# Optimization experiments

Hardware: AMD Instinct MI355X
Metric: run time of the kernel (lower is better)

Reference implementation:

```python
import jax, jax.numpy as jnp
import numpy as np

D_MODEL = 1024
NUM_HEADS = 16
HEAD_DIM = D_MODEL // NUM_HEADS


def setup_inputs() -> dict:
    key = jax.random.key(0)
    k_x, k_wqkv, k_bqkv, k_wout, k_bout = jax.random.split(key, 5)
    B, S = 2, 2048
    x = jax.random.normal(k_x, (B, S, D_MODEL), dtype=jnp.float32)
    # haiku Linear: y = x @ W + b, W shape [in, out]
    init_scale = 1.0 / np.sqrt(D_MODEL)
    W_qkv = jax.random.normal(k_wqkv, (D_MODEL, 3 * D_MODEL), dtype=jnp.float32) * init_scale
    b_qkv = jnp.zeros((3 * D_MODEL,), dtype=jnp.float32)
    W_out = jax.random.normal(k_wout, (D_MODEL, D_MODEL), dtype=jnp.float32) * init_scale
    b_out = jnp.zeros((D_MODEL,), dtype=jnp.float32)
    return {"x": x, "W_qkv": W_qkv, "b_qkv": b_qkv, "W_out": W_out, "b_out": b_out}


def reference(x, W_qkv, b_qkv, W_out, b_out):
    B, S, _ = x.shape
    qkv = x @ W_qkv + b_qkv                      # [B, S, 3*D]
    q, k, v = jnp.split(qkv, 3, axis=-1)         # each [B, S, D]
    # [B, S, D] -> [B, H, S, Hd]
    def heads(t):
        return t.reshape(B, S, NUM_HEADS, HEAD_DIM).transpose(0, 2, 1, 3)
    q, k, v = heads(q), heads(k), heads(v)
    scale = jnp.sqrt(jnp.float32(HEAD_DIM)).astype(x.dtype)
    attn = jnp.einsum('bhqd,bhkd->bhqk', q, k) / scale   # [B, H, S, S]
    attn = jax.nn.softmax(attn, axis=-1)
    out = jnp.einsum('bhqk,bhkd->bhqd', attn, v)          # [B, H, S, Hd]
    out = out.transpose(0, 2, 1, 3).reshape(B, S, D_MODEL)
    return out @ W_out + b_out
```

## Files before the change

### kernel.cpp

```cpp
#include <hip/hip_runtime.h>
#include <stdint.h>


#define BATCH 2
#define SEQ 2048
#define DM 1024
#define NH 16
#define HD 64
#define M_TOT 4096
#define QSCALE 0.18033688011112042f

typedef __bf16 bf16x8 __attribute__((ext_vector_type(8)));
typedef __bf16 bf16x4 __attribute__((ext_vector_type(4)));
typedef float  f32x4  __attribute__((ext_vector_type(4)));

__device__ __forceinline__ void gld_lds16(const void* g, void* l) {
    __builtin_amdgcn_global_load_lds(
        (const __attribute__((address_space(1))) uint32_t*)g,
        (__attribute__((address_space(3))) uint32_t*)l, 16, 0, 0);
}

__device__ __forceinline__ int swz(int r, int c) {
    return r * 64 + ((((c >> 3) ^ (r & 7))) << 3) + (c & 7);
}

__launch_bounds__(256)
__global__ void prep_kernel(const float* __restrict__ x,
                            const float* __restrict__ Wqkv,
                            const float* __restrict__ Wout,
                            __bf16* __restrict__ xs,
                            __bf16* __restrict__ wqt,
                            __bf16* __restrict__ wot)
{
    __shared__ float T[64][69];
    const int tid = threadIdx.x;
    const int blk = blockIdx.x;

    if (blk < 4096) {
        const int i  = blk * 256 + tid;
        const int m  = i >> 8;
        const int c4 = (i & 255) * 4;
        float4 v = *reinterpret_cast<const float4*>(&x[(size_t)m * DM + c4]);
        float a[4] = {v.x, v.y, v.z, v.w};
        bf16x4 hi, lo;
        #pragma unroll
        for (int j = 0; j < 4; ++j) {
            __bf16 h = (__bf16)a[j];
            hi[j] = h;
            lo[j] = (__bf16)(a[j] - (float)h);
        }
        *reinterpret_cast<bf16x4*>(&xs[(size_t)m * (2*DM) + c4]) = hi;
        *reinterpret_cast<bf16x4*>(&xs[(size_t)m * (2*DM) + DM + c4]) = lo;
        return;
    }

    const int bb = (blk < 4864) ? blk - 4096 : blk - 4864;
    const float* W = (blk < 4864) ? Wqkv : Wout;
    __bf16* Wt     = (blk < 4864) ? wqt  : wot;
    const int N    = (blk < 4864) ? 3 * DM : DM;
    const int k0 = (bb & 15) * 64, n0 = (bb >> 4) * 64;

    {
        const int kr = tid >> 4, c4 = (tid & 15) * 4;
        #pragma unroll
        for (int i = 0; i < 4; ++i) {
            float4 v = *reinterpret_cast<const float4*>(
                &W[(size_t)(k0 + kr + 16 * i) * N + n0 + c4]);
            *reinterpret_cast<float4*>(&T[kr + 16 * i][c4]) = v;
        }
    }
    __syncthreads();
    {
        const int n = tid >> 2, kc = (tid & 3) * 16;
        __bf16 hi[16], lo[16];
        #pragma unroll
        for (int j = 0; j < 16; ++j) {
            float v = T[kc + j][n];
            __bf16 h = (__bf16)v;
            hi[j] = h;
            lo[j] = (__bf16)(v - (float)h);
        }
        const size_t ro = (size_t)(n0 + n) * (2*DM) + k0 + kc;
        *reinterpret_cast<bf16x8*>(&Wt[ro])          = *reinterpret_cast<bf16x8*>(&hi[0]);
        *reinterpret_cast<bf16x8*>(&Wt[ro + 8])      = *reinterpret_cast<bf16x8*>(&hi[8]);
        *reinterpret_cast<bf16x8*>(&Wt[ro + DM])     = *reinterpret_cast<bf16x8*>(&lo[0]);
        *reinterpret_cast<bf16x8*>(&Wt[ro + DM + 8]) = *reinterpret_cast<bf16x8*>(&lo[8]);
    }
}

__launch_bounds__(256)
__global__ void gemm_qkv_kernel(const __bf16* __restrict__ A,
                                const __bf16* __restrict__ Bt,
                                const float* __restrict__ bias,
                                __bf16* __restrict__ qs,
                                __bf16* __restrict__ khi_g,
                                __bf16* __restrict__ klo_g,
                                __bf16* __restrict__ vt_g)
{
    __shared__ __align__(16) __bf16 pool[18432];
    __bf16* As = pool;
    __bf16* Bs = pool + 4096;

    const int tid  = threadIdx.x;
    const int w    = tid >> 6;
    const int lane = tid & 63;
    const int n16  = lane & 15;
    const int quad = lane >> 4;
    const int bm = blockIdx.x * 128, bn = blockIdx.y * 128;
    const int wm = (w & 1) * 64,     wn = (w >> 1) * 64;

    const int srow = tid >> 2, sc = (tid & 3) * 8;
    const __bf16* Ar = A  + (size_t)(bm + srow) * (2*DM) + sc;
    const __bf16* Br = Bt + (size_t)(bn + srow) * (2*DM) + sc;

    f32x4 acc[4][4] = {};

    for (int kb = 0; kb < 3 * DM; kb += 32) {
        const int a_k = (kb < DM)     ? kb : kb - DM;
        const int b_k = (kb < 2 * DM) ? kb : kb - 2 * DM;
        __syncthreads();
        gld_lds16(Ar + a_k,                    &As[(size_t)tid * 8]);
        gld_lds16(Ar + a_k + (size_t)64*2*DM,  &As[(size_t)(256 + tid) * 8]);
        gld_lds16(Br + b_k,                    &Bs[(size_t)tid * 8]);
        gld_lds16(Br + b_k + (size_t)64*2*DM,  &Bs[(size_t)(256 + tid) * 8]);
        __syncthreads();

        bf16x8 af[4], bfr[4];
        #pragma unroll
        for (int i = 0; i < 4; ++i)
            af[i] = *reinterpret_cast<const bf16x8*>(&As[(wm + i*16 + n16) * 32 + quad * 8]);
        #pragma unroll
        for (int j = 0; j < 4; ++j)
            bfr[j] = *reinterpret_cast<const bf16x8*>(&Bs[(wn + j*16 + n16) * 32 + quad * 8]);
        #pragma unroll
        for (int i = 0; i < 4; ++i)
            #pragma unroll
            for (int j = 0; j < 4; ++j)
                acc[i][j] = __builtin_amdgcn_mfma_f32_16x16x32_bf16(af[i], bfr[j], acc[i][j], 0, 0, 0);
    }

    const int colb = bn + wn;
    const int part = colb >> 10;
    const int hh   = (colb & 1023) >> 6;
    const int brow = bm + wm;
    const int b    = brow >> 11;
    const int s0   = brow & 2047;
    const int bh   = b * NH + hh;
    const int kt   = s0 >> 6;
    const size_t tb = ((size_t)bh * 32 + kt) * 4096;

    float bv[4];
    #pragma unroll
    for (int j = 0; j < 4; ++j) bv[j] = bias[colb + j * 16 + n16];

    __bf16* scrH = pool + w * 4608;
    __bf16* scrL = scrH + 2304;
    const int lr = lane & 31, hc = lane >> 5;

    __syncthreads();

    #pragma unroll
    for (int p = 0; p < 2; ++p) {
        if (part == 2) {
            #pragma unroll
            for (int jj = 0; jj < 2; ++jj) {
                const int j = 2 * p + jj;
                #pragma unroll
                for (int i = 0; i < 4; ++i) {
                    bf16x4 v4;
                    #pragma unroll
                    for (int r = 0; r < 4; ++r)
                        v4[r] = (__bf16)(acc[i][j][r] + bv[j]);
                    *reinterpret_cast<bf16x4*>(
                        &scrH[(jj * 16 + n16) * 72 + i * 16 + quad * 4]) = v4;
                }
            }
        } else {
            #pragma unroll
            for (int ii = 0; ii < 2; ++ii) {
                const int i = 2 * p + ii;
                #pragma unroll
                for (int j = 0; j < 4; ++j) {
                    #pragma unroll
                    for (int r = 0; r < 4; ++r) {
                        float val = acc[i][j][r] + bv[j];
                        if (part == 0) val *= QSCALE;
                        __bf16 h = (__bf16)val;
                        const int so = (ii * 16 + quad * 4 + r) * 72 + j * 16 + n16;
                        scrH[so] = h;
                        scrL[so] = (__bf16)(val - (float)h);
                    }
                }
            }
        }
        __syncthreads();

        if (part == 0) {
            const size_t qbase = ((size_t)bh * SEQ + s0 + 32 * p + lr) * 128;
            #pragma unroll
            for (int t = 0; t < 4; ++t) {
                const int ch = hc * 4 + t;
                *reinterpret_cast<bf16x8*>(&qs[qbase + ch * 8]) =
                    *reinterpret_cast<const bf16x8*>(&scrH[lr * 72 + ch * 8]);
                *reinterpret_cast<bf16x8*>(&qs[qbase + 64 + ch * 8]) =
                    *reinterpret_cast<const bf16x8*>(&scrL[lr * 72 + ch * 8]);
            }
        } else if (part == 1) {
            const int kr = 32 * p + lr;
            #pragma unroll
            for (int t = 0; t < 4; ++t) {
                const int ch = hc * 4 + t;
                const int src = (ch ^ (lr & 7)) * 8;
                *reinterpret_cast<bf16x8*>(&khi_g[tb + kr * 64 + ch * 8]) =
                    *reinterpret_cast<const bf16x8*>(&scrH[lr * 72 + src]);
                *reinterpret_cast<bf16x8*>(&klo_g[tb + kr * 64 + ch * 8]) =
                    *reinterpret_cast<const bf16x8*>(&scrL[lr * 72 + src]);
            }
        } else {
            const int d = 32 * p + lr;
            #pragma unroll
            for (int t = 0; t < 4; ++t) {
                const int ch = hc * 4 + t;
                const int src = (ch ^ (lr & 7)) * 8;
                *reinterpret_cast<bf16x8*>(&vt_g[tb + d * 64 + ch * 8]) =
                    *reinterpret_cast<const bf16x8*>(&scrH[lr * 72 + src]);
            }
        }
        __syncthreads();
    }
}

__launch_bounds__(256)
__global__ void gemm_out_kernel(const __bf16* __restrict__ A,
                                const __bf16* __restrict__ Bt,
                                const float* __restrict__ bias,
                                float* __restrict__ out)
{
    __shared__ __align__(16) __bf16 AsH[128 * 32];
    __shared__ __align__(16) __bf16 AsL[128 * 32];
    __shared__ __align__(16) __bf16 BsH[64 * 32];
    __shared__ __align__(16) __bf16 BsL[64 * 32];

    const int tid  = threadIdx.x;
    const int w    = tid >> 6;
    const int lane = tid & 63;
    const int n16  = lane & 15;
    const int quad = lane >> 4;
    const int bm = blockIdx.x * 128, bn = blockIdx.y * 64;
    const int wm = (w & 1) * 64,     wn = (w >> 1) * 32;

    const int srow = tid >> 2, sc = (tid & 3) * 8;
    const __bf16* Ar = A  + (size_t)(bm + srow) * (2*DM) + sc;
    const __bf16* Br = Bt + (size_t)(bn + srow) * (2*DM) + sc;

    f32x4 acc[4][2] = {};

    for (int k0 = 0; k0 < DM; k0 += 32) {
        __syncthreads();
        gld_lds16(Ar + k0,                         &AsH[(size_t)tid * 8]);
        gld_lds16(Ar + k0 + (size_t)64*2*DM,       &AsH[(size_t)(256 + tid) * 8]);
        gld_lds16(Ar + DM + k0,                    &AsL[(size_t)tid * 8]);
        gld_lds16(Ar + DM + k0 + (size_t)64*2*DM,  &AsL[(size_t)(256 + tid) * 8]);
        gld_lds16(Br + k0,                         &BsH[(size_t)tid * 8]);
        gld_lds16(Br + DM + k0,                    &BsL[(size_t)tid * 8]);
        __syncthreads();

        bf16x8 afh[4], afl[4], bfh[2], bfl[2];
        #pragma unroll
        for (int i = 0; i < 4; ++i) {
            const int ro = (wm + i*16 + n16) * 32 + quad * 8;
            afh[i] = *reinterpret_cast<const bf16x8*>(&AsH[ro]);
            afl[i] = *reinterpret_cast<const bf16x8*>(&AsL[ro]);
        }
        #pragma unroll
        for (int j = 0; j < 2; ++j) {
            const int ro = (wn + j*16 + n16) * 32 + quad * 8;
            bfh[j] = *reinterpret_cast<const bf16x8*>(&BsH[ro]);
            bfl[j] = *reinterpret_cast<const bf16x8*>(&BsL[ro]);
        }
        #pragma unroll
        for (int i = 0; i < 4; ++i)
            #pragma unroll
            for (int j = 0; j < 2; ++j) {
                acc[i][j] = __builtin_amdgcn_mfma_f32_16x16x32_bf16(afh[i], bfh[j], acc[i][j], 0, 0, 0);
                acc[i][j] = __builtin_amdgcn_mfma_f32_16x16x32_bf16(afh[i], bfl[j], acc[i][j], 0, 0, 0);
                acc[i][j] = __builtin_amdgcn_mfma_f32_16x16x32_bf16(afl[i], bfh[j], acc[i][j], 0, 0, 0);
            }
    }

    #pragma unroll
    for (int j = 0; j < 2; ++j) {
        const int col = bn + wn + j * 16 + n16;
        const float bvv = bias[col];
        #pragma unroll
        for (int i = 0; i < 4; ++i) {
            const int row0 = bm + wm + i * 16 + quad * 4;
            #pragma unroll
            for (int r = 0; r < 4; ++r)
                out[(size_t)(row0 + r) * DM + col] = acc[i][j][r] + bvv;
        }
    }
}

__launch_bounds__(256, 2)
__global__ void flash_attn_v5_kernel(const __bf16* __restrict__ qs,
                                     const __bf16* __restrict__ khi_g,
                                     const __bf16* __restrict__ klo_g,
                                     const __bf16* __restrict__ vt_g,
                                     __bf16* __restrict__ ctx2)
{
    __shared__ __align__(16) __bf16 Khi[2][4096];
    __shared__ __align__(16) __bf16 Klo[2][4096];
    __shared__ __align__(16) __bf16 Vt [2][4096];
    __shared__ __align__(16) __bf16 Ps [8192];

    const int tid  = threadIdx.x;
    const int w    = tid >> 6;
    const int lane = tid & 63;
    const int n16  = lane & 15;
    const int quad = lane >> 4;
    const int bid  = blockIdx.x;
    const int bh = (bid & 7) * 4 + (bid >> 7);
    const int qt = (bid >> 3) & 15;

    bf16x8 qh[2][2], ql[2][2];
    #pragma unroll
    for (int qg = 0; qg < 2; ++qg) {
        const size_t qrow =
            ((size_t)bh * SEQ + qt * 128 + w * 32 + qg * 16 + n16) * 128;
        #pragma unroll
        for (int s2 = 0; s2 < 2; ++s2) {
            qh[qg][s2] = *reinterpret_cast<const bf16x8*>(&qs[qrow + s2 * 32 + quad * 8]);
            ql[qg][s2] = *reinterpret_cast<const bf16x8*>(&qs[qrow + 64 + s2 * 32 + quad * 8]);
        }
    }

    f32x4 o[2][4] = {};
    float l_lane[2] = {};

    for (int kt2 = 0; kt2 < 16; ++kt2) {
        __syncthreads();
        {
            const int buf = w >> 1;
            const size_t tb = ((size_t)bh * 32 + kt2 * 2 + buf) * 4096;
            #pragma unroll
            for (int t = 0; t < 12; ++t) {
                const int rem = (w & 1) * 12 + t;
                const int arr = rem >> 3, sub = rem & 7;
                const int eo = sub * 512 + lane * 8;
                const __bf16* g = (arr == 0 ? khi_g : arr == 1 ? klo_g : vt_g) + tb + eo;
                __bf16* l = (arr == 0 ? Khi[buf] : arr == 1 ? Klo[buf] : Vt[buf]) + eo;
                gld_lds16(g, l);
            }
        }
        __syncthreads();

        #pragma unroll
        for (int hf = 0; hf < 2; ++hf) {
            const __bf16* KhiB = Khi[hf];
            const __bf16* KloB = Klo[hf];
            const __bf16* VtB  = Vt[hf];

            #pragma unroll
            for (int kg = 0; kg < 4; ++kg) {
                const int r = kg * 16 + n16;
                const int o0 = r * 64 + ((quad ^ (r & 7)) << 3);
                const int o1 = r * 64 + (((4 + quad) ^ (r & 7)) << 3);
                bf16x8 kh0 = *reinterpret_cast<const bf16x8*>(&KhiB[o0]);
                bf16x8 kl0 = *reinterpret_cast<const bf16x8*>(&KloB[o0]);
                bf16x8 kh1 = *reinterpret_cast<const bf16x8*>(&KhiB[o1]);
                bf16x8 kl1 = *reinterpret_cast<const bf16x8*>(&KloB[o1]);
                #pragma unroll
                for (int qg = 0; qg < 2; ++qg) {
                    f32x4 sa = {}, sb = {};
                    sa = __builtin_amdgcn_mfma_f32_16x16x32_bf16(kh0, qh[qg][0], sa, 0, 0, 0);
                    sb = __builtin_amdgcn_mfma_f32_16x16x32_bf16(kh1, qh[qg][1], sb, 0, 0, 0);
                    sa = __builtin_amdgcn_mfma_f32_16x16x32_bf16(kl0, qh[qg][0], sa, 0, 0, 0);
                    sb = __builtin_amdgcn_mfma_f32_16x16x32_bf16(kl1, qh[qg][1], sb, 0, 0, 0);
                    sa = __builtin_amdgcn_mfma_f32_16x16x32_bf16(kh0, ql[qg][0], sa, 0, 0, 0);
                    sb = __builtin_amdgcn_mfma_f32_16x16x32_bf16(kh1, ql[qg][1], sb, 0, 0, 0);
                    f32x4 st = sa + sb;

                    f32x4 pp;
                    #pragma unroll
                    for (int r2 = 0; r2 < 4; ++r2) pp[r2] = exp2f(st[r2]);
                    l_lane[qg] += (pp[0] + pp[1]) + (pp[2] + pp[3]);

                    bf16x4 p4;
                    #pragma unroll
                    for (int r2 = 0; r2 < 4; ++r2) p4[r2] = (__bf16)pp[r2];
                    const int prow = w * 32 + qg * 16 + n16;
                    const int ch2 = kg * 2 + (quad >> 1);
                    const int off = prow * 64 + ((ch2 ^ (prow & 7)) << 3) + (quad & 1) * 4;
                    *reinterpret_cast<bf16x4*>(&Ps[off]) = p4;
                }
            }

            bf16x8 pa[2][2];
            #pragma unroll
            for (int qg = 0; qg < 2; ++qg) {
                const int prow = w * 32 + qg * 16 + n16;
                #pragma unroll
                for (int s2 = 0; s2 < 2; ++s2)
                    pa[qg][s2] = *reinterpret_cast<const bf16x8*>(
                        &Ps[prow * 64 + (((s2 * 4 + quad) ^ (prow & 7)) << 3)]);
            }
            #pragma unroll
            for (int c = 0; c < 4; ++c) {
                const int vr = c * 16 + n16;
                bf16x8 vb0 = *reinterpret_cast<const bf16x8*>(
                    &VtB[vr * 64 + ((quad ^ (vr & 7)) << 3)]);
                bf16x8 vb1 = *reinterpret_cast<const bf16x8*>(
                    &VtB[vr * 64 + (((4 + quad) ^ (vr & 7)) << 3)]);
                #pragma unroll
                for (int qg = 0; qg < 2; ++qg) {
                    o[qg][c] = __builtin_amdgcn_mfma_f32_16x16x32_bf16(pa[qg][0], vb0, o[qg][c], 0, 0, 0);
                    o[qg][c] = __builtin_amdgcn_mfma_f32_16x16x32_bf16(pa[qg][1], vb1, o[qg][c], 0, 0, 0);
                }
            }
        }
    }

    #pragma unroll
    for (int qg = 0; qg < 2; ++qg) {
        l_lane[qg] += __shfl_xor(l_lane[qg], 16, 64);
        l_lane[qg] += __shfl_xor(l_lane[qg], 32, 64);
    }

    const int b = bh >> 4, hh = bh & 15;
    #pragma unroll
    for (int qg = 0; qg < 2; ++qg) {
        #pragma unroll
        for (int r2 = 0; r2 < 4; ++r2) {
            const float l = __shfl(l_lane[qg], (quad << 4) + quad * 4 + r2, 64);
            const float linv = 1.0f / l;
            const int srow = qt * 128 + w * 32 + qg * 16 + quad * 4 + r2;
            const size_t rowoff = (size_t)(b * SEQ + srow) * (2*DM);
            #pragma unroll
            for (int c = 0; c < 4; ++c) {
                const int col = hh * HD + c * 16 + n16;
                float v = o[qg][c][r2] * linv;
                __bf16 h = (__bf16)v;
                ctx2[rowoff + col] = h;
                ctx2[rowoff + DM + col] = (__bf16)(v - (float)h);
            }
        }
    }
}

extern "C" void kernel_launch(void* const* d_in, const int* in_sizes, int n_in,
                              void* d_out, int out_size, void* d_ws, size_t ws_size,
                              hipStream_t stream)
{
    const float* x    = (const float*)d_in[0];
    const float* Wqkv = (const float*)d_in[1];
    const float* bqkv = (const float*)d_in[2];
    const float* Wout = (const float*)d_in[3];
    const float* bout = (const float*)d_in[4];
    float* out = (float*)d_out;

    char* ws = (char*)d_ws;
    __bf16* xs   = (__bf16*)(ws);
    __bf16* ctx2 = xs;
    __bf16* wqt  = (__bf16*)(ws + (size_t)16 * 1024 * 1024);
    __bf16* wot  = (__bf16*)(ws + (size_t)28 * 1024 * 1024);
    __bf16* qsb  = (__bf16*)(ws + (size_t)32 * 1024 * 1024);
    __bf16* khi  = (__bf16*)(ws + (size_t)48 * 1024 * 1024);
    __bf16* klo  = (__bf16*)(ws + (size_t)56 * 1024 * 1024);
    __bf16* vt   = (__bf16*)(ws + (size_t)64 * 1024 * 1024);

    prep_kernel<<<dim3(5120), 256, 0, stream>>>(x, Wqkv, Wout, xs, wqt, wot);
    gemm_qkv_kernel<<<dim3(M_TOT / 128, (3 * DM) / 128), 256, 0, stream>>>(
        xs, wqt, bqkv, qsb, khi, klo, vt);
    flash_attn_v5_kernel<<<dim3(512), 256, 0, stream>>>(qsb, khi, klo, vt, ctx2);
    gemm_out_kernel<<<dim3(M_TOT / 128, DM / 64), 256, 0, stream>>>(
        ctx2, wot, bout, out);
}
```

Before: 290.8 us.

## Restructure QKV GEMM into 256x256 tiles with double-buffered pipelined loads

```diff
diff --git a/kernel.cpp b/kernel.cpp
--- a/kernel.cpp
+++ b/kernel.cpp
@@ -18,10 +18,6 @@
     __builtin_amdgcn_global_load_lds(
         (const __attribute__((address_space(1))) uint32_t*)g,
         (__attribute__((address_space(3))) uint32_t*)l, 16, 0, 0);
-}
-
-__device__ __forceinline__ int swz(int r, int c) {
-    return r * 64 + ((((c >> 3) ^ (r & 7))) << 3) + (c & 7);
 }
 
 __launch_bounds__(256)
@@ -88,7 +84,7 @@
     }
 }
 
-__launch_bounds__(256)
+__launch_bounds__(512, 2)
 __global__ void gemm_qkv_kernel(const __bf16* __restrict__ A,
                                 const __bf16* __restrict__ Bt,
                                 const float* __restrict__ bias,
@@ -97,57 +93,143 @@
                                 __bf16* __restrict__ klo_g,
                                 __bf16* __restrict__ vt_g)
 {
-    __shared__ __align__(16) __bf16 pool[18432];
-    __bf16* As = pool;
-    __bf16* Bs = pool + 4096;
+    __shared__ __align__(16) __bf16 pool[65536];
 
     const int tid  = threadIdx.x;
     const int w    = tid >> 6;
     const int lane = tid & 63;
     const int n16  = lane & 15;
     const int quad = lane >> 4;
-    const int bm = blockIdx.x * 128, bn = blockIdx.y * 128;
-    const int wm = (w & 1) * 64,     wn = (w >> 1) * 64;
-
-    const int srow = tid >> 2, sc = (tid & 3) * 8;
-    const __bf16* Ar = A  + (size_t)(bm + srow) * (2*DM) + sc;
-    const __bf16* Br = Bt + (size_t)(bn + srow) * (2*DM) + sc;
-
-    f32x4 acc[4][4] = {};
-
-    for (int kb = 0; kb < 3 * DM; kb += 32) {
-        const int a_k = (kb < DM)     ? kb : kb - DM;
-        const int b_k = (kb < 2 * DM) ? kb : kb - 2 * DM;
-        __syncthreads();
-        gld_lds16(Ar + a_k,                    &As[(size_t)tid * 8]);
-        gld_lds16(Ar + a_k + (size_t)64*2*DM,  &As[(size_t)(256 + tid) * 8]);
-        gld_lds16(Br + b_k,                    &Bs[(size_t)tid * 8]);
-        gld_lds16(Br + b_k + (size_t)64*2*DM,  &Bs[(size_t)(256 + tid) * 8]);
-        __syncthreads();
-
-        bf16x8 af[4], bfr[4];
+
+    const int wg = (blockIdx.x & 7) * 24 + (blockIdx.x >> 3);
+    const int bm = (wg & 15) * 256;
+    const int bn = (wg >> 4) * 256;
+
+    const int wm = (w >> 2) * 128;
+    const int wn = (w & 3) * 64;
+
+    const int r0 = tid >> 3;
+    const int c0 = ((tid & 7) ^ (r0 & 7));
+
+    auto stage = [&](int p, int kcol, int nbuf) {
+        __bf16* dst = pool + nbuf * 32768 + p * 8192;
+        const __bf16* gsrc = (p < 2)
+            ? A  + (size_t)(bm + p * 128) * (2*DM) + kcol
+            : Bt + (size_t)(bn + (p - 2) * 128) * (2*DM) + kcol;
+        gld_lds16(gsrc + (size_t)r0 * (2*DM) + c0 * 8,        dst + (size_t)tid * 8);
+        gld_lds16(gsrc + (size_t)(r0 + 64) * (2*DM) + c0 * 8, dst + (size_t)(512 + tid) * 8);
+    };
+
+    const int rowA = (wm + n16) * 64;
+    const int rowB = (wn + n16) * 64;
+    const int sx0 = ((quad)     ^ (n16 & 7)) << 3;
+    const int sx1 = ((4 + quad) ^ (n16 & 7)) << 3;
+
+    f32x4 acc[8][4] = {};
+    bf16x8 af[4][2], bf0[2][2], bf1[2][2];
+
+    stage(0, 0, 0); stage(1, 0, 0); stage(2, 0, 0); stage(3, 0, 0);
+
+    #pragma unroll 2
+    for (int t = 0; t < 48; ++t) {
+        const int buf = t & 1;
+        const __bf16* bufA = pool + buf * 32768;
+        const __bf16* bufB = bufA + 16384;
+        const int nbuf = buf ^ 1;
+        const bool pre = (t < 47);
+        const int tt = t + 1;
+        const int a_k = (tt < 16) ? tt * 64 : tt * 64 - DM;
+        const int b_k = (tt < 32) ? tt * 64 : tt * 64 - 2 * DM;
+
+        if (pre) {
+            stage(0, a_k, nbuf);
+            asm volatile("s_waitcnt vmcnt(2)" ::: "memory");
+        } else {
+            asm volatile("s_waitcnt vmcnt(0)" ::: "memory");
+        }
+        __builtin_amdgcn_s_barrier();
+        __builtin_amdgcn_sched_barrier(0);
+        #pragma unroll
+        for (int i = 0; i < 4; ++i) {
+            af[i][0] = *reinterpret_cast<const bf16x8*>(bufA + rowA + i * 1024 + sx0);
+            af[i][1] = *reinterpret_cast<const bf16x8*>(bufA + rowA + i * 1024 + sx1);
+        }
+        #pragma unroll
+        for (int j = 0; j < 2; ++j) {
+            bf0[j][0] = *reinterpret_cast<const bf16x8*>(bufB + rowB + j * 1024 + sx0);
+            bf0[j][1] = *reinterpret_cast<const bf16x8*>(bufB + rowB + j * 1024 + sx1);
+        }
+        asm volatile("s_waitcnt lgkmcnt(0)" ::: "memory");
+        __builtin_amdgcn_sched_barrier(0);
+        __builtin_amdgcn_s_setprio(1);
         #pragma unroll
         for (int i = 0; i < 4; ++i)
-            af[i] = *reinterpret_cast<const bf16x8*>(&As[(wm + i*16 + n16) * 32 + quad * 8]);
-        #pragma unroll
-        for (int j = 0; j < 4; ++j)
-            bfr[j] = *reinterpret_cast<const bf16x8*>(&Bs[(wn + j*16 + n16) * 32 + quad * 8]);
+            #pragma unroll
+            for (int j = 0; j < 2; ++j) {
+                acc[i][j] = __builtin_amdgcn_mfma_f32_16x16x32_bf16(af[i][0], bf0[j][0], acc[i][j], 0, 0, 0);
+                acc[i][j] = __builtin_amdgcn_mfma_f32_16x16x32_bf16(af[i][1], bf0[j][1], acc[i][j], 0, 0, 0);
+            }
+        __builtin_amdgcn_s_setprio(0);
+
+        #pragma unroll
+        for (int j = 0; j < 2; ++j) {
+            bf1[j][0] = *reinterpret_cast<const bf16x8*>(bufB + rowB + (2 + j) * 1024 + sx0);
+            bf1[j][1] = *reinterpret_cast<const bf16x8*>(bufB + rowB + (2 + j) * 1024 + sx1);
+        }
+        if (pre) stage(1, a_k, nbuf);
+        __builtin_amdgcn_s_barrier();
+        __builtin_amdgcn_sched_barrier(0);
+        asm volatile("s_waitcnt lgkmcnt(0)" ::: "memory");
+        __builtin_amdgcn_sched_barrier(0);
+        __builtin_amdgcn_s_setprio(1);
         #pragma unroll
         for (int i = 0; i < 4; ++i)
             #pragma unroll
-            for (int j = 0; j < 4; ++j)
-                acc[i][j] = __builtin_amdgcn_mfma_f32_16x16x32_bf16(af[i], bfr[j], acc[i][j], 0, 0, 0);
-    }
+            for (int j = 0; j < 2; ++j) {
+                acc[i][2 + j] = __builtin_amdgcn_mfma_f32_16x16x32_bf16(af[i][0], bf1[j][0], acc[i][2 + j], 0, 0, 0);
+                acc[i][2 + j] = __builtin_amdgcn_mfma_f32_16x16x32_bf16(af[i][1], bf1[j][1], acc[i][2 + j], 0, 0, 0);
+            }
+        __builtin_amdgcn_s_setprio(0);
+
+        #pragma unroll
+        for (int i = 0; i < 4; ++i) {
+            af[i][0] = *reinterpret_cast<const bf16x8*>(bufA + rowA + (4 + i) * 1024 + sx0);
+            af[i][1] = *reinterpret_cast<const bf16x8*>(bufA + rowA + (4 + i) * 1024 + sx1);
+        }
+        if (pre) stage(2, b_k, nbuf);
+        __builtin_amdgcn_s_barrier();
+        __builtin_amdgcn_sched_barrier(0);
+        asm volatile("s_waitcnt lgkmcnt(0)" ::: "memory");
+        __builtin_amdgcn_sched_barrier(0);
+        __builtin_amdgcn_s_setprio(1);
+        #pragma unroll
+        for (int i = 0; i < 4; ++i)
+            #pragma unroll
+            for (int j = 0; j < 2; ++j) {
+                acc[4 + i][j] = __builtin_amdgcn_mfma_f32_16x16x32_bf16(af[i][0], bf0[j][0], acc[4 + i][j], 0, 0, 0);
+                acc[4 + i][j] = __builtin_amdgcn_mfma_f32_16x16x32_bf16(af[i][1], bf0[j][1], acc[4 + i][j], 0, 0, 0);
+            }
+        __builtin_amdgcn_s_setprio(0);
+
+        if (pre) stage(3, b_k, nbuf);
+        __builtin_amdgcn_s_barrier();
+        __builtin_amdgcn_sched_barrier(0);
+        __builtin_amdgcn_s_setprio(1);
+        #pragma unroll
+        for (int i = 0; i < 4; ++i)
+            #pragma unroll
+            for (int j = 0; j < 2; ++j) {
+                acc[4 + i][2 + j] = __builtin_amdgcn_mfma_f32_16x16x32_bf16(af[i][0], bf1[j][0], acc[4 + i][2 + j], 0, 0, 0);
+                acc[4 + i][2 + j] = __builtin_amdgcn_mfma_f32_16x16x32_bf16(af[i][1], bf1[j][1], acc[4 + i][2 + j], 0, 0, 0);
+            }
+        __builtin_amdgcn_s_setprio(0);
+    }
+
+    __syncthreads();
 
     const int colb = bn + wn;
     const int part = colb >> 10;
     const int hh   = (colb & 1023) >> 6;
-    const int brow = bm + wm;
-    const int b    = brow >> 11;
-    const int s0   = brow & 2047;
-    const int bh   = b * NH + hh;
-    const int kt   = s0 >> 6;
-    const size_t tb = ((size_t)bh * 32 + kt) * 4096;
 
     float bv[4];
     #pragma unroll
@@ -157,76 +239,84 @@
     __bf16* scrL = scrH + 2304;
     const int lr = lane & 31, hc = lane >> 5;
 
-    __syncthreads();
-
     #pragma unroll
-    for (int p = 0; p < 2; ++p) {
-        if (part == 2) {
-            #pragma unroll
-            for (int jj = 0; jj < 2; ++jj) {
-                const int j = 2 * p + jj;
-                #pragma unroll
-                for (int i = 0; i < 4; ++i) {
-                    bf16x4 v4;
+    for (int mi = 0; mi < 2; ++mi) {
+        const int brow = bm + wm + mi * 64;
+        const int b    = brow >> 11;
+        const int s0   = brow & 2047;
+        const int bh   = b * NH + hh;
+        const int kt   = s0 >> 6;
+        const size_t tb = ((size_t)bh * 32 + kt) * 4096;
+
+        #pragma unroll
+        for (int p = 0; p < 2; ++p) {
+            if (part == 2) {
+                #pragma unroll
+                for (int jj = 0; jj < 2; ++jj) {
+                    const int j = 2 * p + jj;
                     #pragma unroll
-                    for (int r = 0; r < 4; ++r)
-                        v4[r] = (__bf16)(acc[i][j][r] + bv[j]);
-                    *reinterpret_cast<bf16x4*>(
-                        &scrH[(jj * 16 + n16) * 72 + i * 16 + quad * 4]) = v4;
-                }
-            }
-        } else {
-            #pragma unroll
-            for (int ii = 0; ii < 2; ++ii) {
-                const int i = 2 * p + ii;
-                #pragma unroll
-                for (int j = 0; j < 4; ++j) {
+                    for (int i = 0; i < 4; ++i) {
+                        bf16x4 v4;
+                        #pragma unroll
+                        for (int r = 0; r < 4; ++r)
+                            v4[r] = (__bf16)(acc[4 * mi + i][j][r] + bv[j]);
+                        *reinterpret_cast<bf16x4*>(
+                            &scrH[(jj * 16 + n16) * 72 + i * 16 + quad * 4]) = v4;
+                    }
+                }
+            } else {
+                #pragma unroll
+                for (int ii = 0; ii < 2; ++ii) {
+                    const int i = 2 * p + ii;
                     #pragma unroll
-                    for (int r = 0; r < 4; ++r) {
-                        float val = acc[i][j][r] + bv[j];
-                        if (part == 0) val *= QSCALE;
-                        __bf16 h = (__bf16)val;
-                        const int so = (ii * 16 + quad * 4 + r) * 72 + j * 16 + n16;
-                        scrH[so] = h;
-                        scrL[so] = (__bf16)(val - (float)h);
+                    for (int j = 0; j < 4; ++j) {
+                        #pragma unroll
+                        for (int r = 0; r < 4; ++r) {
+                            float val = acc[4 * mi + i][j][r] + bv[j];
+                            if (part == 0) val *= QSCALE;
+                            __bf16 h = (__bf16)val;
+                            const int so = (ii * 16 + quad * 4 + r) * 72 + j * 16 + n16;
+                            scrH[so] = h;
+                            scrL[so] = (__bf16)(val - (float)h);
+                        }
                     }
                 }
             }
-        }
-        __syncthreads();
-
-        if (part == 0) {
-            const size_t qbase = ((size_t)bh * SEQ + s0 + 32 * p + lr) * 128;
-            #pragma unroll
-            for (int t = 0; t < 4; ++t) {
-                const int ch = hc * 4 + t;
-                *reinterpret_cast<bf16x8*>(&qs[qbase + ch * 8]) =
-                    *reinterpret_cast<const bf16x8*>(&scrH[lr * 72 + ch * 8]);
-                *reinterpret_cast<bf16x8*>(&qs[qbase + 64 + ch * 8]) =
-                    *reinterpret_cast<const bf16x8*>(&scrL[lr * 72 + ch * 8]);
-            }
-        } else if (part == 1) {
-            const int kr = 32 * p + lr;
-            #pragma unroll
-            for (int t = 0; t < 4; ++t) {
-                const int ch = hc * 4 + t;
-                const int src = (ch ^ (lr & 7)) * 8;
-                *reinterpret_cast<bf16x8*>(&khi_g[tb + kr * 64 + ch * 8]) =
-                    *reinterpret_cast<const bf16x8*>(&scrH[lr * 72 + src]);
-                *reinterpret_cast<bf16x8*>(&klo_g[tb + kr * 64 + ch * 8]) =
-                    *reinterpret_cast<const bf16x8*>(&scrL[lr * 72 + src]);
-            }
-        } else {
-            const int d = 32 * p + lr;
-            #pragma unroll
-            for (int t = 0; t < 4; ++t) {
-                const int ch = hc * 4 + t;
-                const int src = (ch ^ (lr & 7)) * 8;
-                *reinterpret_cast<bf16x8*>(&vt_g[tb + d * 64 + ch * 8]) =
-                    *reinterpret_cast<const bf16x8*>(&scrH[lr * 72 + src]);
-            }
-        }
-        __syncthreads();
+            __syncthreads();
+
+            if (part == 0) {
+                const size_t qbase = ((size_t)bh * SEQ + s0 + 32 * p + lr) * 128;
+                #pragma unroll
+                for (int t = 0; t < 4; ++t) {
+                    const int ch = hc * 4 + t;
+                    *reinterpret_cast<bf16x8*>(&qs[qbase + ch * 8]) =
+                        *reinterpret_cast<const bf16x8*>(&scrH[lr * 72 + ch * 8]);
+                    *reinterpret_cast<bf16x8*>(&qs[qbase + 64 + ch * 8]) =
+                        *reinterpret_cast<const bf16x8*>(&scrL[lr * 72 + ch * 8]);
+                }
+            } else if (part == 1) {
+                const int kr = 32 * p + lr;
+                #pragma unroll
+                for (int t = 0; t < 4; ++t) {
+                    const int ch = hc * 4 + t;
+                    const int src = (ch ^ (lr & 7)) * 8;
+                    *reinterpret_cast<bf16x8*>(&khi_g[tb + kr * 64 + ch * 8]) =
+                        *reinterpret_cast<const bf16x8*>(&scrH[lr * 72 + src]);
+                    *reinterpret_cast<bf16x8*>(&klo_g[tb + kr * 64 + ch * 8]) =
+                        *reinterpret_cast<const bf16x8*>(&scrL[lr * 72 + src]);
+                }
+            } else {
+                const int d = 32 * p + lr;
+                #pragma unroll
+                for (int t = 0; t < 4; ++t) {
+                    const int ch = hc * 4 + t;
+                    const int src = (ch ^ (lr & 7)) * 8;
+                    *reinterpret_cast<bf16x8*>(&vt_g[tb + d * 64 + ch * 8]) =
+                        *reinterpret_cast<const bf16x8*>(&scrH[lr * 72 + src]);
+                }
+            }
+            __syncthreads();
+        }
     }
 }
 
@@ -470,7 +560,7 @@
     __bf16* vt   = (__bf16*)(ws + (size_t)64 * 1024 * 1024);
 
     prep_kernel<<<dim3(5120), 256, 0, stream>>>(x, Wqkv, Wout, xs, wqt, wot);
-    gemm_qkv_kernel<<<dim3(M_TOT / 128, (3 * DM) / 128), 256, 0, stream>>>(
+    gemm_qkv_kernel<<<dim3(192), 512, 0, stream>>>(
         xs, wqt, bqkv, qsb, khi, klo, vt);
     flash_attn_v5_kernel<<<dim3(512), 256, 0, stream>>>(qsb, khi, klo, vt, ctx2);
     gemm_out_kernel<<<dim3(M_TOT / 128, DM / 64), 256, 0, stream>>>(
```

Result: faster. 284.0 us (-2.3%).
